# Kernel tuning notes

Measured on AMD Instinct MI355X. Metric: run time of the kernel, lower is better.

## Reference

```python
import jax, jax.numpy as jnp
import numpy as np

STEP = 16
LEAK = 32
KSIZE = STEP + LEAK          # 48
PAD = 32                     # ceil((48+16)/2)
THETA = 25.6                 # dense(0.05) * synapses(512) * input_channel(1)
FODEP = 48                   # = kernel_size
BIAS = 0.5
OUT_CH = 1


def setup_inputs() -> dict:
    key = jax.random.key(0)
    k1, k2 = jax.random.split(key, 2)
    input_spikes = (jax.random.uniform(k1, (16, 1, 512, 512)) < 0.05).astype(jnp.float32)
    # weight ~ Exponential(rate=1/w_init) with w_init=0.5, clipped to [0,1]
    u = jax.random.uniform(k2, (1024, 512), minval=1e-6, maxval=1.0)
    weight = jnp.clip(-0.5 * jnp.log(u), 0.0, 1.0)
    return {"input_spikes": input_spikes, "weight": weight}


def _winner_takes_all(potentials):
    # potentials: [B, C, N, T] -> iterate over time with sequential depression state
    p = jnp.transpose(potentials, (3, 1, 0, 2))  # [T, C, B, N]
    T, C, B, N = p.shape

    def step(dep, p_t):
        # dep: [C, B, N] depression counters (integer-valued floats)
        wins = []
        for c in range(C):
            pot = p_t[c] * (dep[c] == 0)                      # mask depressed neurons
            widx = jnp.argmax(pot, axis=-1)                   # [B]
            wval = jnp.take_along_axis(pot, widx[:, None], axis=-1)[:, 0]
            spike = (wval > THETA).astype(pot.dtype)          # [B]
            win = jax.nn.one_hot(widx, N, dtype=pot.dtype) * spike[:, None]  # [B, N]
            # torch: scatter_add(-spike*fodep at winner) then += spike*fodep broadcast
            dep = dep.at[c].add(spike[:, None] * FODEP - win * FODEP)
            # torch: depression += winners[t, c] * fodep (all channels)
            dep = dep + win[None] * FODEP
            wins.append(win)
        dep = jnp.clip(dep - 1.0, 0.0, FODEP - 1.0)
        return dep, jnp.stack(wins, 0)                        # [C, B, N]

    dep0 = jnp.zeros((C, B, N), p.dtype)
    _, winners = jax.lax.scan(step, dep0, p)                  # winners: [T, C, B, N]
    return jnp.transpose(winners, (2, 1, 3, 0))               # [B, C, N, T]


def _forward(input_spikes, weight):
    B, Ci, S, T = input_spikes.shape
    x = input_spikes.reshape(B, Ci * S, T)
    # StepFireLeak.get_weight_kernel
    t = jnp.arange(KSIZE, dtype=weight.dtype)                 # [K]
    t_spike = t / STEP                                        # [K]
    t_leak = -(t - weight[..., None] * STEP) / LEAK + weight[..., None]  # [O, I, K]
    kernel = jnp.maximum(0.0, jnp.minimum(t_spike, t_leak))[..., ::-1]   # [O, I, K] flipped
    pot = jax.lax.conv_general_dilated(
        x, kernel, window_strides=(1,), padding=[(PAD, PAD)],
        dimension_numbers=('NCH', 'OIH', 'NCH'))              # [B, O*N, T']
    N = weight.shape[0] // OUT_CH
    pot = pot.reshape(B, OUT_CH, N, -1) + BIAS * THETA        # labels=None branch
    return _winner_takes_all(pot)


def reference(input_spikes, weight):
    return _forward(input_spikes, weight)
```

## Files before the change

kernel.cpp:

```cpp
#include <hip/hip_runtime.h>
#include <stdint.h>


#define NB 16
#define NI 512
#define NT 512
#define NO 1024
#define TOUT 529
#define SCAP 96
#define OTILE 4
#define PLANE 570
#define THETA_F 25.6f
#define BIAS_T 12.8f

__global__ __launch_bounds__(256) void k_spikes(const float* __restrict__ x,
                                                unsigned short* __restrict__ slist,
                                                unsigned int* __restrict__ spkw,
                                                unsigned int* __restrict__ counts,
                                                float* __restrict__ hg) {
    __shared__ unsigned short sls[4][SCAP];
    int wq = threadIdx.x >> 6, lane = threadIdx.x & 63;
    int row = blockIdx.x * 4 + wq;
    int b = row >> 9;
    const float* xr = x + (size_t)row * NT;
    for (int j = lane; j < SCAP; j += 64) sls[wq][j] = 0x1FFF;
    int base = 0;
    for (int kk = 0; kk < 8; ++kk) {
        int t = kk * 64 + lane;
        bool pred = xr[t] > 0.5f;
        unsigned long long mask = __ballot(pred);
        int pre = __popcll(mask & ((1ull << lane) - 1ull));
        int pos = base + pre;
        if (pred) {
            if (pos < SCAP) sls[wq][pos] = (unsigned short)t;
            unsafeAtomicAdd(&hg[b * NT + t], 1.0f);
        }
        base += __popcll(mask);
    }
    __syncthreads();
    if (lane < SCAP / 2) {
        unsigned v = (unsigned)sls[wq][2 * lane] | ((unsigned)sls[wq][2 * lane + 1] << 16);
        ((unsigned int*)(slist + (size_t)row * SCAP))[lane] = v;
    }
    if (lane < 32)
        spkw[(size_t)row * 32 + lane] =
            ((unsigned)sls[wq][lane] << 3) | ((unsigned)sls[wq][lane + 32] << 19);
    if (lane == 0) counts[row] = (unsigned)min(base, SCAP);
}

__device__ __forceinline__ float kval(float b15, int tau) {
    if (tau > 47) return 0.f;
    float f = (float)tau * 0.0625f;
    float g = b15 - (float)tau * 0.03125f;
    return fmaxf(0.f, fminf(f, g));
}

__global__ __launch_bounds__(256) void k_taps(const float* __restrict__ weight,
                                              float4* __restrict__ tap) {
    int p = blockIdx.x * 256 + threadIdx.x;
    int o = p >> 9, i = p & 511;
    float w = weight[o * NI + i];
    float b15 = 1.5f * w;
    float vA1 = 0.f, vA2 = 0.f, vB1 = 0.f, vB2 = 0.f;
    int posA = 2048, posB = 2048, state = 0;
    int n1 = (int)floorf(16.0f * w);
    int n2 = (int)floorf(48.0f * w);
    int lo1 = max(n1, 1);
    int hi1, lo2, hi2;
    if (n2 <= n1 + 4) { hi1 = min(n2 + 3, 49); lo2 = 1; hi2 = 0; }
    else             { hi1 = min(n1 + 3, 49); lo2 = n2; hi2 = min(n2 + 3, 49); }

#define TAPRUN(LO, HI)                                                                \
    {                                                                                 \
        float Km1 = kval(b15, (LO) - 1), Km2 = kval(b15, (LO) - 2);                   \
        for (int tau = (LO); tau <= (HI); ++tau) {                                    \
            float K = kval(b15, tau);                                                 \
            float d = (K - Km1) - (Km1 - Km2);                                        \
            if (tau == 1) d -= 0.0625f;                       \
            if (d != 0.f) {                                                           \
                if (state == 0)      { posA = tau; vA1 = d; state = 1; }              \
                else if (state == 1) { if (tau == posA + 1) { vA2 = d; state = 2; }   \
                                       else { posB = tau; vB1 = d; state = 3; } }     \
                else if (state == 2) { posB = tau; vB1 = d; state = 3; }              \
                else if (state == 3) { if (tau == posB + 1) { vB2 = d; state = 4; } } \
            }                                                                         \
            Km2 = Km1; Km1 = K;                                                       \
        }                                                                             \
    }
    TAPRUN(lo1, hi1)
    if (lo2 <= hi2) TAPRUN(lo2, hi2)

    size_t base = 2 * ((size_t)o * NI + i);
    tap[base]     = make_float4(vA1, vA2, __int_as_float(posA >= 2048 ? 16384 : posA * 8), 0.f);
    tap[base + 1] = make_float4(vB1, vB2, __int_as_float(posB >= 2048 ? 16384 : posB * 8), 0.f);
}

#define PROC(TP, WV, CNT, IDX)                                                        \
    {                                                                                 \
        const int p8 = __float_as_int((TP).z);                                        \
        {                                                                             \
            int e8 = min((int)((WV) & 0xFFFFu) + p8, dcap8);                          \
            float2* cell = (float2*)((char*)accw + e8);                               \
            float2 v = *cell; v.x += (TP).x; v.y += (TP).y; *cell = v;                \
        }                                                                             \
        if ((CNT) > 32u) {                                                            \
            int e8 = min((int)((WV) >> 16) + p8, dcap8);                              \
            float2* cell = (float2*)((char*)accw + e8);                               \
            float2 v = *cell; v.x += (TP).x; v.y += (TP).y; *cell = v;                \
        }                                                                             \
        if ((CNT) > 64u) {                                                            \
            const unsigned short* sr = slist + (size_t)(b * NI + (IDX)) * SCAP;       \
            for (int kk = 64 + k; kk < (int)(CNT); kk += 32) {                        \
                int e8 = min(((int)sr[kk] << 3) + p8, dcap8);                         \
                float2* cell = (float2*)((char*)accw + e8);                           \
                float2 v = *cell; v.x += (TP).x; v.y += (TP).y; *cell = v;            \
            }                                                                         \
        }                                                                             \
    }

__global__ __launch_bounds__(256, 4) void k_scatter(const unsigned short* __restrict__ slist,
                                                    const unsigned int* __restrict__ spkw,
                                                    const unsigned int* __restrict__ counts,
                                                    const float4* __restrict__ tap,
                                                    const float* __restrict__ hg,
                                                    float* __restrict__ pot) {
    __shared__ __align__(16) float2 acc[OTILE * 2 * PLANE];
    __shared__ double pub[512];
    const int o0 = blockIdx.x * OTILE;
    const int b  = blockIdx.y;
    const int tid = threadIdx.x;
    const int w = tid >> 6, lane = tid & 63;
    const int k = lane >> 1, ramp = lane & 1;
    const int dcap8 = (561 + (k & 7)) * 8;

    for (int idx = tid; idx < OTILE * PLANE; idx += 256)
        ((float4*)acc)[idx] = make_float4(0.f, 0.f, 0.f, 0.f);
    __syncthreads();

    float2* accw = acc + (w * 2 + ramp) * PLANE;
    const unsigned int* wrow = spkw + (size_t)(b * NI) * 32 + k;
    const float4* trow = tap + 2 * (size_t)(o0 + w) * NI + ramp;
    const uint4* crow = (const uint4*)(counts + b * NI);

    float4 ntA = trow[0], ntB = trow[2], ntC = trow[4], ntD = trow[6];
    unsigned nwA = wrow[0], nwB = wrow[32], nwC = wrow[64], nwD = wrow[96];
    uint4 ncc = crow[0];

    const int NIQ = NI / 4;
    for (int iq = 0; iq < NIQ; ++iq) {
        const float4 tA = ntA, tB = ntB, tC = ntC, tD = ntD;
        const unsigned wA = nwA, wB = nwB, wC = nwC, wD = nwD;
        const uint4 cc = ncc;
        if (iq + 1 < NIQ) {
            const float4* tb = trow + (size_t)(iq + 1) * 8;
            ntA = tb[0]; ntB = tb[2]; ntC = tb[4]; ntD = tb[6];
            const unsigned int* wb = wrow + (size_t)(iq + 1) * 128;
            nwA = wb[0]; nwB = wb[32]; nwC = wb[64]; nwD = wb[96];
            ncc = crow[iq + 1];
        }
        const int i0 = iq * 4;
        PROC(tA, wA, cc.x, i0)
        PROC(tB, wB, cc.y, i0 + 1)
        PROC(tC, wC, cc.z, i0 + 2)
        PROC(tD, wD, cc.w, i0 + 3)
    }
    __syncthreads();

    const int q = lane;
    const float2* pr0 = acc + (w * 2) * PLANE;
    const float2* pr1 = pr0 + PLANE;
    const float* hb = hg + b * NT;
    double dsv[9];
    double s1d = 0.0, s2d = 0.0;
#pragma unroll
    for (int r = 0; r < 9; ++r) {
        int e = q * 9 + r;
        double d = 0.0;
        if (e < 561) {
            float2 c0 = pr0[e], c1 = pr1[e];
            d = (double)c0.x + (double)c1.x;
            if (e >= 1) {
                float2 m0 = pr0[e - 1], m1 = pr1[e - 1];
                d += (double)m0.y + (double)m1.y;
                if (e <= 512) d += 0.0625 * (double)hb[e - 1];
            }
        }
        dsv[r] = d; s1d += d; s2d += s1d;
    }
    pub[2 * tid] = s1d; pub[2 * tid + 1] = s2d;
    __syncthreads();
    if (tid < 4) {
        double c1 = 0.0, c2 = 0.0;
        for (int qq = 0; qq < 64; ++qq) {
            int j = (tid << 6) + qq;
            double S1 = pub[2 * j], S2 = pub[2 * j + 1];
            pub[2 * j] = c1; pub[2 * j + 1] = c2;
            c2 += 9.0 * c1 + S2;
            c1 += S1;
        }
    }
    __syncthreads();
    {
        const double C1 = pub[2 * tid], C2 = pub[2 * tid + 1];
        double a1 = 0.0, a2 = 0.0;
        float2* rowW = acc + (w * 2) * PLANE;
#pragma unroll
        for (int r = 0; r < 9; ++r) {
            a1 += dsv[r]; a2 += a1;
            int e = q * 9 + r;
            if (e < 561) rowW[e].x = (float)(C2 + C1 * (double)(r + 1) + a2);
        }
    }
    __syncthreads();
    for (int oo = 0; oo < OTILE; ++oo)
        for (int t = tid; t < TOUT; t += 256)
            pot[((size_t)(b * NO + o0 + oo)) * TOUT + t] = acc[(oo * 2) * PLANE + t + 15].x + BIAS_T;
}

__global__ __launch_bounds__(256) void k_argmax1(const float* __restrict__ pot,
                                                 float* __restrict__ pval,
                                                 unsigned short* __restrict__ pidx) {
    __shared__ float sv[4][64];
    __shared__ int   si[4][64];
    int b = blockIdx.y, c = blockIdx.z;
    int lane = threadIdx.x & 63, grp = threadIdx.x >> 6;
    int t = blockIdx.x * 64 + lane;
    bool valid = t < TOUT;
    float best = -1.f; int bidx = 0;
    if (valid) {
        int ob = c * 128 + grp * 32;
        for (int od = 0; od < 32; ++od) {
            int o = ob + od;
            float v = pot[((size_t)(b * NO + o)) * TOUT + t];
            if (v > best) { best = v; bidx = o; }
        }
    }
    sv[grp][lane] = best; si[grp][lane] = bidx;
    __syncthreads();
    if (grp == 0 && valid) {
#pragma unroll
        for (int g = 1; g < 4; ++g) {
            float v = sv[g][lane];
            if (v > best) { best = v; bidx = si[g][lane]; }
        }
        pval[((size_t)(c * NB + b)) * TOUT + t] = best;
        pidx[((size_t)(c * NB + b)) * TOUT + t] = (unsigned short)bidx;
    }
}

__global__ __launch_bounds__(64) void k_argmax2(const float* __restrict__ pval,
                                                const unsigned short* __restrict__ pidx,
                                                float* __restrict__ aval,
                                                unsigned short* __restrict__ aidx) {
    int b = blockIdx.y;
    int t = blockIdx.x * 64 + threadIdx.x;
    if (t >= TOUT) return;
    float best = -1.f; int bidx = 0;
#pragma unroll
    for (int c = 0; c < 8; ++c) {
        size_t idx = ((size_t)(c * NB + b)) * TOUT + t;
        float v = pval[idx];
        if (v > best) { best = v; bidx = pidx[idx]; }
    }
    aval[t * NB + b] = best;
    aidx[t * NB + b] = (unsigned short)bidx;
}

__global__ __launch_bounds__(256) void k_wta(const float* __restrict__ aval,
                                             const unsigned short* __restrict__ aidx,
                                             float* __restrict__ out) {
    __shared__ float lv[TOUT * NB];
    __shared__ unsigned short li[TOUT * NB];
    for (int idx = threadIdx.x; idx < TOUT * NB; idx += 256) { lv[idx] = aval[idx]; li[idx] = aidx[idx]; }
    __syncthreads();
    int b = threadIdx.x;
    if (b < NB) {
        int r = 0;
        for (int t = 0; t < TOUT; ++t) {
            float v = lv[t * NB + b];
            if (r == 0 && v > THETA_F) {
                int n = (int)li[t * NB + b];
                out[((size_t)(b * NO + n)) * TOUT + t] = 1.0f;
                r = 48;
            }
            r = max(r - 1, 0);
        }
    }
}

extern "C" void kernel_launch(void* const* d_in, const int* in_sizes, int n_in,
                              void* d_out, int out_size, void* d_ws, size_t ws_size,
                              hipStream_t stream) {
    const float* x      = (const float*)d_in[0];
    const float* weight = (const float*)d_in[1];
    float* out = (float*)d_out;
    char* ws = (char*)d_ws;
    unsigned short* slist  = (unsigned short*)(ws);
    unsigned int*   spkw   = (unsigned int*)(ws + 1572864);
    unsigned int*   counts = (unsigned int*)(ws + 2621440);
    float4*         tap    = (float4*)(ws + 2654208);
    float*          hg     = (float*)(ws + 19431424);
    float*          aval   = (float*)(ws + 19464192);
    unsigned short* aidx   = (unsigned short*)(ws + 19498048);
    float*          pval   = (float*)(ws + 19514976);
    unsigned short* pidx   = (unsigned short*)(ws + 19785824);

    hipMemsetAsync(hg, 0, NB * NT * sizeof(float), stream);
    k_spikes<<<2048, 256, 0, stream>>>(x, slist, spkw, counts, hg);
    k_taps<<<2048, 256, 0, stream>>>(weight, tap);
    k_scatter<<<dim3(NO / OTILE, NB), 256, 0, stream>>>(slist, spkw, counts, tap, hg, out);
    k_argmax1<<<dim3(9, NB, 8), 256, 0, stream>>>(out, pval, pidx);
    k_argmax2<<<dim3(9, NB), 64, 0, stream>>>(pval, pidx, aval, aidx);
    hipMemsetAsync(d_out, 0, (size_t)out_size * sizeof(float), stream);
    k_wta<<<1, 256, 0, stream>>>(aval, aidx, out);
}
```

Before: 490.2 us.

## Fuse argmax into scatter epilogue via packed 64-bit atomicMax

Instead of writing the full potential tensor to global memory and reducing it with two argmax kernels, the scatter kernel now reduces its four output neurons per time step in shared memory. It then publishes a packed (value, inverted index) key with a 64-bit atomicMax into a small per-(t, b) buffer. This removes a large write and re-read of the potential tensor (about 35 MB) and two kernel launches. The cost is global atomic contention (256 blocks per address) and reliance on positive floats ordering correctly as unsigned bits, with the inverted index keeping ties on the lowest neuron.

Result: no change. 499.6 us (+1.9%).

```diff
diff --git a/kernel.cpp b/kernel.cpp
--- a/kernel.cpp
+++ b/kernel.cpp
@@ -123,7 +123,7 @@
                                                     const unsigned int* __restrict__ counts,
                                                     const float4* __restrict__ tap,
                                                     const float* __restrict__ hg,
-                                                    float* __restrict__ pot) {
+                                                    unsigned long long* __restrict__ pm) {
     __shared__ __align__(16) float2 acc[OTILE * 2 * PLANE];
     __shared__ double pub[512];
     const int o0 = blockIdx.x * OTILE;
@@ -212,66 +212,30 @@
         }
     }
     __syncthreads();
-    for (int oo = 0; oo < OTILE; ++oo)
-        for (int t = tid; t < TOUT; t += 256)
-            pot[((size_t)(b * NO + o0 + oo)) * TOUT + t] = acc[(oo * 2) * PLANE + t + 15].x + BIAS_T;
-}
-
-__global__ __launch_bounds__(256) void k_argmax1(const float* __restrict__ pot,
-                                                 float* __restrict__ pval,
-                                                 unsigned short* __restrict__ pidx) {
-    __shared__ float sv[4][64];
-    __shared__ int   si[4][64];
-    int b = blockIdx.y, c = blockIdx.z;
-    int lane = threadIdx.x & 63, grp = threadIdx.x >> 6;
-    int t = blockIdx.x * 64 + lane;
-    bool valid = t < TOUT;
-    float best = -1.f; int bidx = 0;
-    if (valid) {
-        int ob = c * 128 + grp * 32;
-        for (int od = 0; od < 32; ++od) {
-            int o = ob + od;
-            float v = pot[((size_t)(b * NO + o)) * TOUT + t];
-            if (v > best) { best = v; bidx = o; }
-        }
-    }
-    sv[grp][lane] = best; si[grp][lane] = bidx;
-    __syncthreads();
-    if (grp == 0 && valid) {
+    for (int t = tid; t < TOUT; t += 256) {
+        float best = acc[t + 15].x;
+        int bo = 0;
 #pragma unroll
-        for (int g = 1; g < 4; ++g) {
-            float v = sv[g][lane];
-            if (v > best) { best = v; bidx = si[g][lane]; }
-        }
-        pval[((size_t)(c * NB + b)) * TOUT + t] = best;
-        pidx[((size_t)(c * NB + b)) * TOUT + t] = (unsigned short)bidx;
-    }
-}
-
-__global__ __launch_bounds__(64) void k_argmax2(const float* __restrict__ pval,
-                                                const unsigned short* __restrict__ pidx,
-                                                float* __restrict__ aval,
-                                                unsigned short* __restrict__ aidx) {
-    int b = blockIdx.y;
-    int t = blockIdx.x * 64 + threadIdx.x;
-    if (t >= TOUT) return;
-    float best = -1.f; int bidx = 0;
-#pragma unroll
-    for (int c = 0; c < 8; ++c) {
-        size_t idx = ((size_t)(c * NB + b)) * TOUT + t;
-        float v = pval[idx];
-        if (v > best) { best = v; bidx = pidx[idx]; }
-    }
-    aval[t * NB + b] = best;
-    aidx[t * NB + b] = (unsigned short)bidx;
-}
-
-__global__ __launch_bounds__(256) void k_wta(const float* __restrict__ aval,
-                                             const unsigned short* __restrict__ aidx,
+        for (int oo = 1; oo < OTILE; ++oo) {
+            float v = acc[(oo * 2) * PLANE + t + 15].x;
+            if (v > best) { best = v; bo = oo; }
+        }
+        best += BIAS_T;
+        unsigned long long key = ((unsigned long long)__float_as_uint(best) << 32)
+                               | (unsigned)(NO - 1 - (o0 + bo));
+        atomicMax(pm + (size_t)t * NB + b, key);
+    }
+}
+
+__global__ __launch_bounds__(256) void k_wta(const unsigned long long* __restrict__ pm,
                                              float* __restrict__ out) {
     __shared__ float lv[TOUT * NB];
     __shared__ unsigned short li[TOUT * NB];
-    for (int idx = threadIdx.x; idx < TOUT * NB; idx += 256) { lv[idx] = aval[idx]; li[idx] = aidx[idx]; }
+    for (int idx = threadIdx.x; idx < TOUT * NB; idx += 256) {
+        unsigned long long key = pm[idx];
+        lv[idx] = __uint_as_float((unsigned)(key >> 32));
+        li[idx] = (unsigned short)(NO - 1 - (int)(key & 0xFFFFFFFFu));
+    }
     __syncthreads();
     int b = threadIdx.x;
     if (b < NB) {
@@ -300,17 +264,13 @@
     unsigned int*   counts = (unsigned int*)(ws + 2621440);
     float4*         tap    = (float4*)(ws + 2654208);
     float*          hg     = (float*)(ws + 19431424);
-    float*          aval   = (float*)(ws + 19464192);
-    unsigned short* aidx   = (unsigned short*)(ws + 19498048);
-    float*          pval   = (float*)(ws + 19514976);
-    unsigned short* pidx   = (unsigned short*)(ws + 19785824);
+    unsigned long long* pm = (unsigned long long*)(ws + 19464192);
 
     hipMemsetAsync(hg, 0, NB * NT * sizeof(float), stream);
+    hipMemsetAsync(pm, 0, TOUT * NB * sizeof(unsigned long long), stream);
+    hipMemsetAsync(d_out, 0, (size_t)out_size * sizeof(float), stream);
     k_spikes<<<2048, 256, 0, stream>>>(x, slist, spkw, counts, hg);
     k_taps<<<2048, 256, 0, stream>>>(weight, tap);
-    k_scatter<<<dim3(NO / OTILE, NB), 256, 0, stream>>>(slist, spkw, counts, tap, hg, out);
-    k_argmax1<<<dim3(9, NB, 8), 256, 0, stream>>>(out, pval, pidx);
-    k_argmax2<<<dim3(9, NB), 64, 0, stream>>>(pval, pidx, aval, aidx);
-    hipMemsetAsync(d_out, 0, (size_t)out_size * sizeof(float), stream);
-    k_wta<<<1, 256, 0, stream>>>(aval, aidx, out);
-}
+    k_scatter<<<dim3(NO / OTILE, NB), 256, 0, stream>>>(slist, spkw, counts, tap, hg, pm);
+    k_wta<<<1, 256, 0, stream>>>(pm, out);
+}
```
